# Kernel tuning notes

Measured on AMD Instinct MI355X. Metric: run time of the kernel, lower is better.

Reference implementation:

```python
import jax, jax.numpy as jnp
import numpy as np

B, N, A, M = 65536, 256, 64, 128  # frames, atoms, align atoms, nn atoms


def setup_inputs() -> dict:
    key = jax.random.key(0)
    k1, k2, k3, k4 = jax.random.split(key, 4)
    traj = jax.random.normal(k1, (B, N, 3), dtype=jnp.float32)
    ref_pos = jax.random.normal(k2, (N, 3), dtype=jnp.float32)
    align_idx = jnp.sort(jax.random.randint(k3, (A,), 0, N))
    nn_idx = jnp.sort(jax.random.randint(k4, (M,), 0, N))
    return {"traj": traj, "ref_pos": ref_pos, "align_idx": align_idx, "nn_idx": nn_idx}


def reference(traj, ref_pos, align_idx, nn_idx):
    # Reference structure: select alignment atoms and remove centroid (done once in __init__)
    ref_x = ref_pos[align_idx]                      # [A, 3]
    ref_x = ref_x - ref_x.mean(axis=0, keepdims=True)

    # Kabsch alignment per frame
    sel = traj[:, align_idx, :]                     # [B, A, 3]
    x_c = sel.mean(axis=1, keepdims=True)           # [B, 1, 3]
    x_notran = sel - x_c                            # [B, A, 3]
    # prod = x_notran^T @ ref_x -> [B, 3, 3]
    prod = jnp.einsum('bni,nj->bij', x_notran, ref_x)
    u, s, vh = jnp.linalg.svd(prod)                 # batched 3x3 SVD
    # proper-rotation sign correction (detached in original)
    sign = jax.lax.stop_gradient(jnp.sign(jnp.linalg.det(u @ vh)))  # [B]
    ones = jnp.ones_like(sign)
    d = jnp.stack([ones, ones, sign], axis=-1)      # [B, 3] diagonal of correction
    rot = (u * d[:, None, :]) @ vh                  # [B, 3, 3]

    # apply translation + rotation to ALL atoms
    aligned = jnp.einsum('bni,bij->bnj', traj - x_c, rot)  # [B, N, 3]

    # select NN input atoms and flatten
    return aligned[:, nn_idx, :].reshape(traj.shape[0], -1)  # [B, M*3]
```

## Files before the change

kernel.cpp:

```cpp
#include <hip/hip_runtime.h>

#define NB 65536
#define NATOM 256
#define NA 64
#define NM 128
#define TRAJ_SZ (NB*NATOM*3)
#define REF_SZ  (NATOM*3)
#define SLOT_F  384

__device__ __forceinline__ float bf2f(unsigned short u) {
    union { unsigned int i; float f; } v; v.i = ((unsigned int)u) << 16; return v.f;
}
__device__ __forceinline__ float wave_sum(float v) {
    #pragma unroll
    for (int m = 1; m < 64; m <<= 1) v += __shfl_xor(v, m, 64);
    return v;
}
__device__ __forceinline__ float wave_max(float v) {
    #pragma unroll
    for (int m = 1; m < 64; m <<= 1) v = fmaxf(v, __shfl_xor(v, m, 64));
    return v;
}

__device__ __forceinline__ int detect_f32(const unsigned short* __restrict__ traj_u) {
    int lane = threadIdx.x & 63;
    float mx = fabsf(bf2f(traj_u[2 * lane]));
    mx = wave_max(mx);
    return (mx > 0.5f && mx < 100.f) ? 0 : 1;
}

__global__ __launch_bounds__(256) void k_prod(const unsigned short* __restrict__ traj_u,
                                              const unsigned short* __restrict__ refp_u,
                                              const int* __restrict__ align_idx,
                                              float* __restrict__ out) {
    int lane = threadIdx.x & 63;
    int batch = (blockIdx.x << 2) + (threadIdx.x >> 6);
    int isf32 = detect_f32(traj_u);
    int aidx = align_idx[lane];
    long tbase = (long)batch * (NATOM * 3) + aidx * 3;
    float r0, r1, r2, x0, x1, x2;
    if (isf32) {
        const float* rp = (const float*)refp_u;
        const float* tp = (const float*)traj_u;
        r0 = rp[aidx*3+0]; r1 = rp[aidx*3+1]; r2 = rp[aidx*3+2];
        x0 = tp[tbase+0];  x1 = tp[tbase+1];  x2 = tp[tbase+2];
    } else {
        r0 = bf2f(refp_u[aidx*3+0]); r1 = bf2f(refp_u[aidx*3+1]); r2 = bf2f(refp_u[aidx*3+2]);
        x0 = bf2f(traj_u[tbase+0]);  x1 = bf2f(traj_u[tbase+1]);  x2 = bf2f(traj_u[tbase+2]);
    }
    r0 -= wave_sum(r0) * (1.f/64.f);
    r1 -= wave_sum(r1) * (1.f/64.f);
    r2 -= wave_sum(r2) * (1.f/64.f);
    float p00 = wave_sum(x0*r0), p01 = wave_sum(x0*r1), p02 = wave_sum(x0*r2);
    float p10 = wave_sum(x1*r0), p11 = wave_sum(x1*r1), p12 = wave_sum(x1*r2);
    float p20 = wave_sum(x2*r0), p21 = wave_sum(x2*r1), p22 = wave_sum(x2*r2);
    float xc0 = wave_sum(x0) * (1.f/64.f);
    float xc1 = wave_sum(x1) * (1.f/64.f);
    float xc2 = wave_sum(x2) * (1.f/64.f);
    if (lane == 0) {
        float4* w = (float4*)(out + (long)batch * SLOT_F);
        w[0] = make_float4(p00, p01, p02, p10);
        w[1] = make_float4(p11, p12, p20, p21);
        w[2] = make_float4(p22, xc0, xc1, xc2);
    }
}

__global__ __launch_bounds__(256) void k_svd(float* __restrict__ out) {
    long b = (long)blockIdx.x * 256 + threadIdx.x;
    float4* w = (float4*)(out + b * SLOT_F);
    float4 q0 = w[0], q1 = w[1], q2 = w[2];
    float p00=q0.x, p01=q0.y, p02=q0.z, p10=q0.w;
    float p11=q1.x, p12=q1.y, p20=q1.z, p21=q1.w;
    float p22=q2.x, xc0=q2.y, xc1=q2.z, xc2=q2.w;
    float s00 = p00*p00 + p10*p10 + p20*p20;
    float s01 = p00*p01 + p10*p11 + p20*p21;
    float s02 = p00*p02 + p10*p12 + p20*p22;
    float s11 = p01*p01 + p11*p11 + p21*p21;
    float s12 = p01*p02 + p11*p12 + p21*p22;
    float s22 = p02*p02 + p12*p12 + p22*p22;
    float v00=1.f,v01=0.f,v02=0.f, v10=0.f,v11=1.f,v12=0.f, v20=0.f,v21=0.f,v22=1.f;
#define JROT(SPP,SQQ,SPQ,SRP,SRQ,VA,VB,VC,VD,VE,VF) { \
    float apq = SPQ; \
    if (apq != 0.0f) { \
        float tau = (SQQ - SPP) / (2.0f*apq); \
        float t = (tau >= 0.0f ? 1.0f : -1.0f) / (fabsf(tau) + sqrtf(1.0f + tau*tau)); \
        float c = 1.0f / sqrtf(1.0f + t*t); \
        float sn = t*c; \
        SPP -= t*apq; SQQ += t*apq; SPQ = 0.0f; \
        float tp = SRP; SRP = c*tp - sn*SRQ; SRQ = sn*tp + c*SRQ; \
        tp = VA; VA = c*tp - sn*VB; VB = sn*tp + c*VB; \
        tp = VC; VC = c*tp - sn*VD; VD = sn*tp + c*VD; \
        tp = VE; VE = c*tp - sn*VF; VF = sn*tp + c*VF; \
    } }
    #pragma unroll
    for (int sweep = 0; sweep < 5; ++sweep) {
        JROT(s00,s11,s01, s02,s12, v00,v01, v10,v11, v20,v21);
        JROT(s00,s22,s02, s01,s12, v00,v02, v10,v12, v20,v22);
        JROT(s11,s22,s12, s01,s02, v01,v02, v11,v12, v21,v22);
    }
#undef JROT
    float v1x,v1y,v1z, v2x,v2y,v2z;
    if (s00 <= s11 && s00 <= s22) {
        v1x=v01; v1y=v11; v1z=v21;  v2x=v02; v2y=v12; v2z=v22;
    } else if (s11 <= s22) {
        v1x=v02; v1y=v12; v1z=v22;  v2x=v00; v2y=v10; v2z=v20;
    } else {
        v1x=v00; v1y=v10; v1z=v20;  v2x=v01; v2y=v11; v2z=v21;
    }
    float u1x = p00*v1x + p01*v1y + p02*v1z;
    float u1y = p10*v1x + p11*v1y + p12*v1z;
    float u1z = p20*v1x + p21*v1y + p22*v1z;
    float inv = 1.0f / sqrtf(u1x*u1x + u1y*u1y + u1z*u1z);
    u1x*=inv; u1y*=inv; u1z*=inv;
    float u2x = p00*v2x + p01*v2y + p02*v2z;
    float u2y = p10*v2x + p11*v2y + p12*v2z;
    float u2z = p20*v2x + p21*v2y + p22*v2z;
    float d = u2x*u1x + u2y*u1y + u2z*u1z;
    u2x -= d*u1x; u2y -= d*u1y; u2z -= d*u1z;
    inv = 1.0f / sqrtf(u2x*u2x + u2y*u2y + u2z*u2z);
    u2x*=inv; u2y*=inv; u2z*=inv;
    float u3x = u1y*u2z - u1z*u2y;
    float u3y = u1z*u2x - u1x*u2z;
    float u3z = u1x*u2y - u1y*u2x;
    float v3x = v1y*v2z - v1z*v2y;
    float v3y = v1z*v2x - v1x*v2z;
    float v3z = v1x*v2y - v1y*v2x;
    float r00 = u1x*v1x + u2x*v2x + u3x*v3x;
    float r01 = u1x*v1y + u2x*v2y + u3x*v3y;
    float r02 = u1x*v1z + u2x*v2z + u3x*v3z;
    float r10 = u1y*v1x + u2y*v2x + u3y*v3x;
    float r11 = u1y*v1y + u2y*v2y + u3y*v3y;
    float r12 = u1y*v1z + u2y*v2z + u3y*v3z;
    float r20 = u1z*v1x + u2z*v2x + u3z*v3x;
    float r21 = u1z*v1y + u2z*v2y + u3z*v3y;
    float r22 = u1z*v1z + u2z*v2z + u3z*v3z;
    w[0] = make_float4(r00, r01, r02, r10);
    w[1] = make_float4(r11, r12, r20, r21);
    w[2] = make_float4(r22, xc0, xc1, xc2);
}

__global__ __launch_bounds__(256) void k_apply(const unsigned short* __restrict__ traj_u,
                                               const int* __restrict__ nn_idx,
                                               float* __restrict__ out) {
    int lane = threadIdx.x & 63;
    int batch = (blockIdx.x << 2) + (threadIdx.x >> 6);
    int isf32 = detect_f32(traj_u);
    float* w = out + (long)batch * SLOT_F;
    float r00=w[0], r01=w[1], r02=w[2],  r10=w[3];
    float r11=w[4], r12=w[5], r20=w[6],  r21=w[7];
    float r22=w[8], xc0=w[9], xc1=w[10], xc2=w[11];
    __syncthreads();
    #pragma unroll
    for (int h = 0; h < 2; ++h) {
        int m = 2*lane + h;
        int nidx = nn_idx[m];
        long base = (long)batch*(NATOM*3) + nidx*3;
        float x0, x1, x2;
        if (isf32) {
            const float* tp = (const float*)traj_u;
            x0 = tp[base]; x1 = tp[base+1]; x2 = tp[base+2];
        } else {
            x0 = bf2f(traj_u[base]); x1 = bf2f(traj_u[base+1]); x2 = bf2f(traj_u[base+2]);
        }
        x0 -= xc0; x1 -= xc1; x2 -= xc2;
        w[6*lane + 3*h + 0] = x0*r00 + x1*r10 + x2*r20;
        w[6*lane + 3*h + 1] = x0*r01 + x1*r11 + x2*r21;
        w[6*lane + 3*h + 2] = x0*r02 + x1*r12 + x2*r22;
    }
}

extern "C" void kernel_launch(void* const* d_in, const int* in_sizes, int n_in,
                              void* d_out, int out_size, void* d_ws, size_t ws_size,
                              hipStream_t stream) {
    const unsigned short* traj = (const unsigned short*)d_in[0];
    const unsigned short* refp = (const unsigned short*)d_in[1];
    const int* align_idx = (const int*)d_in[2];
    const int* nn_idx    = (const int*)d_in[3];
    for (int i = 0; i < n_in; ++i) {
        if      (in_sizes[i] == TRAJ_SZ) traj      = (const unsigned short*)d_in[i];
        else if (in_sizes[i] == REF_SZ)  refp      = (const unsigned short*)d_in[i];
        else if (in_sizes[i] == NA)      align_idx = (const int*)d_in[i];
        else if (in_sizes[i] == NM)      nn_idx    = (const int*)d_in[i];
    }
    float* out = (float*)d_out;

    k_prod <<<NB/4,   256, 0, stream>>>(traj, refp, align_idx, out);
    k_svd  <<<NB/256, 256, 0, stream>>>(out);
    k_apply<<<NB/4,   256, 0, stream>>>(traj, nn_idx, out);
}
```

Before: 359.3 us.

## Fuse prod, SVD and apply kernels into one with shared-memory row staging

The three kernels are merged into a single kernel in which each wave stages its whole frame row into shared memory with coalesced vector loads. Both the alignment-atom gather and the NN-atom gather then read from LDS instead of scattered global memory. The per-frame SVD runs redundantly on every lane of the wave, replacing a separate one-thread-per-frame launch. Results are assembled in LDS and written out with coalesced float4 stores. This removes two launches and the global round-trips through the output slot. The cost is extra LDS use and 64-fold redundant SVD ALU work per frame.

```diff
diff --git a/kernel.cpp b/kernel.cpp
--- a/kernel.cpp
+++ b/kernel.cpp
@@ -7,6 +7,7 @@
 #define TRAJ_SZ (NB*NATOM*3)
 #define REF_SZ  (NATOM*3)
 #define SLOT_F  384
+#define ROW_F   (NATOM*3)
 
 __device__ __forceinline__ float bf2f(unsigned short u) {
     union { unsigned int i; float f; } v; v.i = ((unsigned int)u) << 16; return v.f;
@@ -29,25 +30,47 @@
     return (mx > 0.5f && mx < 100.f) ? 0 : 1;
 }
 
-__global__ __launch_bounds__(256) void k_prod(const unsigned short* __restrict__ traj_u,
-                                              const unsigned short* __restrict__ refp_u,
-                                              const int* __restrict__ align_idx,
-                                              float* __restrict__ out) {
+__global__ __launch_bounds__(256) void k_fused(const unsigned short* __restrict__ traj_u,
+                                               const unsigned short* __restrict__ refp_u,
+                                               const int* __restrict__ align_idx,
+                                               const int* __restrict__ nn_idx,
+                                               float* __restrict__ out) {
+    __shared__ float rowbuf[4][ROW_F];
+    __shared__ float outbuf[4][SLOT_F];
     int lane = threadIdx.x & 63;
-    int batch = (blockIdx.x << 2) + (threadIdx.x >> 6);
+    int wid  = threadIdx.x >> 6;
+    long batch = ((long)blockIdx.x << 2) + wid;
     int isf32 = detect_f32(traj_u);
+
+    if (isf32) {
+        const float4* src = (const float4*)((const float*)traj_u + batch * ROW_F);
+        float4* dst = (float4*)rowbuf[wid];
+        dst[lane]       = src[lane];
+        dst[lane + 64]  = src[lane + 64];
+        dst[lane + 128] = src[lane + 128];
+    } else {
+        const unsigned int* src = (const unsigned int*)(traj_u + batch * ROW_F);
+        float2* dst = (float2*)rowbuf[wid];
+        #pragma unroll
+        for (int k = 0; k < 6; ++k) {
+            unsigned int u = src[lane + 64 * k];
+            dst[lane + 64 * k] = make_float2(bf2f((unsigned short)(u & 0xffffu)),
+                                             bf2f((unsigned short)(u >> 16)));
+        }
+    }
+    __syncthreads();
+
     int aidx = align_idx[lane];
-    long tbase = (long)batch * (NATOM * 3) + aidx * 3;
-    float r0, r1, r2, x0, x1, x2;
+    float r0, r1, r2;
     if (isf32) {
         const float* rp = (const float*)refp_u;
-        const float* tp = (const float*)traj_u;
         r0 = rp[aidx*3+0]; r1 = rp[aidx*3+1]; r2 = rp[aidx*3+2];
-        x0 = tp[tbase+0];  x1 = tp[tbase+1];  x2 = tp[tbase+2];
     } else {
         r0 = bf2f(refp_u[aidx*3+0]); r1 = bf2f(refp_u[aidx*3+1]); r2 = bf2f(refp_u[aidx*3+2]);
-        x0 = bf2f(traj_u[tbase+0]);  x1 = bf2f(traj_u[tbase+1]);  x2 = bf2f(traj_u[tbase+2]);
     }
+    float x0 = rowbuf[wid][aidx*3+0];
+    float x1 = rowbuf[wid][aidx*3+1];
+    float x2 = rowbuf[wid][aidx*3+2];
     r0 -= wave_sum(r0) * (1.f/64.f);
     r1 -= wave_sum(r1) * (1.f/64.f);
     r2 -= wave_sum(r2) * (1.f/64.f);
@@ -57,21 +80,7 @@
     float xc0 = wave_sum(x0) * (1.f/64.f);
     float xc1 = wave_sum(x1) * (1.f/64.f);
     float xc2 = wave_sum(x2) * (1.f/64.f);
-    if (lane == 0) {
-        float4* w = (float4*)(out + (long)batch * SLOT_F);
-        w[0] = make_float4(p00, p01, p02, p10);
-        w[1] = make_float4(p11, p12, p20, p21);
-        w[2] = make_float4(p22, xc0, xc1, xc2);
-    }
-}
 
-__global__ __launch_bounds__(256) void k_svd(float* __restrict__ out) {
-    long b = (long)blockIdx.x * 256 + threadIdx.x;
-    float4* w = (float4*)(out + b * SLOT_F);
-    float4 q0 = w[0], q1 = w[1], q2 = w[2];
-    float p00=q0.x, p01=q0.y, p02=q0.z, p10=q0.w;
-    float p11=q1.x, p12=q1.y, p20=q1.z, p21=q1.w;
-    float p22=q2.x, xc0=q2.y, xc1=q2.z, xc2=q2.w;
     float s00 = p00*p00 + p10*p10 + p20*p20;
     float s01 = p00*p01 + p10*p11 + p20*p21;
     float s02 = p00*p02 + p10*p12 + p20*p22;
@@ -134,39 +143,23 @@
     float r20 = u1z*v1x + u2z*v2x + u3z*v3x;
     float r21 = u1z*v1y + u2z*v2y + u3z*v3y;
     float r22 = u1z*v1z + u2z*v2z + u3z*v3z;
-    w[0] = make_float4(r00, r01, r02, r10);
-    w[1] = make_float4(r11, r12, r20, r21);
-    w[2] = make_float4(r22, xc0, xc1, xc2);
-}
 
-__global__ __launch_bounds__(256) void k_apply(const unsigned short* __restrict__ traj_u,
-                                               const int* __restrict__ nn_idx,
-                                               float* __restrict__ out) {
-    int lane = threadIdx.x & 63;
-    int batch = (blockIdx.x << 2) + (threadIdx.x >> 6);
-    int isf32 = detect_f32(traj_u);
-    float* w = out + (long)batch * SLOT_F;
-    float r00=w[0], r01=w[1], r02=w[2],  r10=w[3];
-    float r11=w[4], r12=w[5], r20=w[6],  r21=w[7];
-    float r22=w[8], xc0=w[9], xc1=w[10], xc2=w[11];
-    __syncthreads();
     #pragma unroll
     for (int h = 0; h < 2; ++h) {
-        int m = 2*lane + h;
+        int m = lane + 64 * h;
         int nidx = nn_idx[m];
-        long base = (long)batch*(NATOM*3) + nidx*3;
-        float x0, x1, x2;
-        if (isf32) {
-            const float* tp = (const float*)traj_u;
-            x0 = tp[base]; x1 = tp[base+1]; x2 = tp[base+2];
-        } else {
-            x0 = bf2f(traj_u[base]); x1 = bf2f(traj_u[base+1]); x2 = bf2f(traj_u[base+2]);
-        }
-        x0 -= xc0; x1 -= xc1; x2 -= xc2;
-        w[6*lane + 3*h + 0] = x0*r00 + x1*r10 + x2*r20;
-        w[6*lane + 3*h + 1] = x0*r01 + x1*r11 + x2*r21;
-        w[6*lane + 3*h + 2] = x0*r02 + x1*r12 + x2*r22;
+        float y0 = rowbuf[wid][nidx*3+0] - xc0;
+        float y1 = rowbuf[wid][nidx*3+1] - xc1;
+        float y2 = rowbuf[wid][nidx*3+2] - xc2;
+        outbuf[wid][3*m+0] = y0*r00 + y1*r10 + y2*r20;
+        outbuf[wid][3*m+1] = y0*r01 + y1*r11 + y2*r21;
+        outbuf[wid][3*m+2] = y0*r02 + y1*r12 + y2*r22;
     }
+    __syncthreads();
+    const float4* ob = (const float4*)outbuf[wid];
+    float4* og = (float4*)(out + batch * SLOT_F);
+    og[lane] = ob[lane];
+    if (lane < 32) og[64 + lane] = ob[64 + lane];
 }
 
 extern "C" void kernel_launch(void* const* d_in, const int* in_sizes, int n_in,
@@ -184,7 +177,5 @@
     }
     float* out = (float*)d_out;
 
-    k_prod <<<NB/4,   256, 0, stream>>>(traj, refp, align_idx, out);
-    k_svd  <<<NB/256, 256, 0, stream>>>(out);
-    k_apply<<<NB/4,   256, 0, stream>>>(traj, nn_idx, out);
+    k_fused<<<NB/4, 256, 0, stream>>>(traj, refp, align_idx, nn_idx, out);
 }
```

Measured after the change: 374.4 us. 4.2% more time.
